# Kernel optimization log

Hardware: AMD Instinct MI355X
Metric: run time of the kernel (lower is better)

Reference implementation:

```python
import jax, jax.numpy as jnp
import numpy as np

B, N, F_IN = 32, 512, 16
H, D_HID, D_OUT = 8, 8, 32
ALPHA = 0.2
NEG = -9e15


def setup_inputs() -> dict:
    key = jax.random.key(0)
    ks = jax.random.split(key, 10)
    xv = jax.random.normal(ks[0], (B, N, F_IN), dtype=jnp.float32)
    adj = (jax.random.uniform(ks[1], (B, N, N)) < 0.05).astype(jnp.float32)
    s = 0.1
    W_heads = jax.random.normal(ks[2], (H, F_IN, D_HID), dtype=jnp.float32) * s
    a1 = jax.random.normal(ks[3], (H, D_HID), dtype=jnp.float32) * s
    a2 = jax.random.normal(ks[4], (H, D_HID), dtype=jnp.float32) * s
    W_out = jax.random.normal(ks[5], (H * D_HID, D_OUT), dtype=jnp.float32) * s
    a1_out = jax.random.normal(ks[6], (D_OUT,), dtype=jnp.float32) * s
    a2_out = jax.random.normal(ks[7], (D_OUT,), dtype=jnp.float32) * s
    W_q = jax.random.normal(ks[8], (N * D_OUT, N), dtype=jnp.float32) * s
    b_q = jax.random.normal(ks[9], (N,), dtype=jnp.float32) * s
    return {"xv": xv, "adj": adj, "W_heads": W_heads, "a1": a1, "a2": a2,
            "W_out": W_out, "a1_out": a1_out, "a2_out": a2_out,
            "W_q": W_q, "b_q": b_q}


def _masked_softmax(e, adj_mask):
    # e: [..., N, N]; adj_mask broadcastable bool
    scores = jnp.where(adj_mask, e, NEG)
    return jax.nn.softmax(scores, axis=-1)


def reference(xv, adj, W_heads, a1, a2, W_out, a1_out, a2_out, W_q, b_q):
    mask = adj > 0  # [B, N, N]
    # --- multi-head GAT layer (vectorized over batch and heads) ---
    Wh = jnp.einsum('bnf,hfd->bhnd', xv, W_heads)            # [B,H,N,Dh]
    f1 = jnp.einsum('bhnd,hd->bhn', Wh, a1)                   # a^T[:Dh] . Wh_i
    f2 = jnp.einsum('bhnd,hd->bhn', Wh, a2)                   # a^T[Dh:] . Wh_j
    e = jax.nn.leaky_relu(f1[:, :, :, None] + f2[:, :, None, :], ALPHA)  # [B,H,N,N]
    att = _masked_softmax(e, mask[:, None, :, :])
    h = jnp.einsum('bhnm,bhmd->bhnd', att, Wh)
    h = jax.nn.elu(h)                                         # concat=True heads apply elu
    h_cat = jnp.transpose(h, (0, 2, 1, 3)).reshape(B, N, H * D_HID)  # head-major concat
    # --- output attention layer (concat=False: no internal elu) ---
    Who = jnp.einsum('bnf,fd->bnd', h_cat, W_out)             # [B,N,Do]
    g1 = Who @ a1_out                                         # [B,N]
    g2 = Who @ a2_out
    eo = jax.nn.leaky_relu(g1[:, :, None] + g2[:, None, :], ALPHA)
    att_o = _masked_softmax(eo, mask)
    out = jnp.einsum('bnm,bmd->bnd', att_o, Who)
    out = jax.nn.elu(out)                                     # F.elu applied in forward
    # --- Q head ---
    q = out.reshape(B, N * D_OUT) @ W_q + b_q                 # [B,N]
    return q[..., None]                                       # [B,N,1]
```

## Files before the change

### kernel.cpp

```cpp
#include <hip/hip_runtime.h>
#include <hip/hip_bf16.h>
#include <stdint.h>


typedef unsigned long long u64;
typedef unsigned short u16;

__device__ __forceinline__ float eluf(float x) { return x > 0.f ? x : __expf(x) - 1.f; }
__device__ __forceinline__ float lrelu(float x) { return fmaxf(x, 0.2f * x); }

__device__ float g_Wh[1048576];
__device__ float g_f1[131072];
__device__ float g_f2[131072];
__device__ u64   g_mask[131072];
__device__ float g_hcat[1048576];
__device__ float g_Who[524288];
__device__ float g_g1[16384];
__device__ float g_g2[16384];
__device__ float g_out2[524288];
__device__ float g_partial[1048576];

__global__ __launch_bounds__(256) void k_mask(const float* __restrict__ adj) {
  int gw = blockIdx.x * 4 + (threadIdx.x >> 6);
  int lane = threadIdx.x & 63;
  float v = adj[(size_t)(gw >> 3) * 512 + (gw & 7) * 64 + lane];
  u64 bal = __ballot(v > 0.f);
  if (lane == 0) g_mask[gw] = bal;
}

__global__ __launch_bounds__(256) void k_wh(const float* __restrict__ xv,
                                            const float* __restrict__ whd,
                                            const float* __restrict__ a1,
                                            const float* __restrict__ a2) {
  __shared__ float w_s[128];
  __shared__ float a1s[8], a2s[8];
  int tid = threadIdx.x;
  int g = blockIdx.x * 256 + tid;
  int h = (g >> 9) & 7;
  if (tid < 128) w_s[tid] = whd[h * 128 + tid];
  if (tid < 8) { a1s[tid] = a1[h * 8 + tid]; a2s[tid] = a2[h * 8 + tid]; }
  __syncthreads();

  int b = g >> 12, n = g & 511;
  const float4* xp = (const float4*)(xv + (size_t)(b * 512 + n) * 16);
  float x[16];
#pragma unroll
  for (int i = 0; i < 4; ++i) {
    float4 v = xp[i];
    x[4 * i] = v.x; x[4 * i + 1] = v.y; x[4 * i + 2] = v.z; x[4 * i + 3] = v.w;
  }

  float wh[8] = {0, 0, 0, 0, 0, 0, 0, 0};
#pragma unroll
  for (int f = 0; f < 16; ++f) {
    float xf = x[f];
#pragma unroll
    for (int d = 0; d < 8; ++d) wh[d] += xf * w_s[f * 8 + d];
  }
  float s1 = 0.f, s2 = 0.f;
#pragma unroll
  for (int d = 0; d < 8; ++d) { s1 += wh[d] * a1s[d]; s2 += wh[d] * a2s[d]; }

  float* dst = g_Wh + (size_t)g * 8;
  *(float4*)dst = make_float4(wh[0], wh[1], wh[2], wh[3]);
  *(float4*)(dst + 4) = make_float4(wh[4], wh[5], wh[6], wh[7]);
  g_f1[g] = s1;
  g_f2[g] = s2;
}

__global__ __launch_bounds__(512) void k_gat() {
  __shared__ float wh_s[4096];
  __shared__ float f2s[512];

  int bh = blockIdx.x;
  int b = bh >> 3, h = bh & 7;
  int tid = threadIdx.x;

  {
    const float4* src = (const float4*)(g_Wh + (size_t)bh * 4096);
    float4* dst = (float4*)wh_s;
    dst[tid] = src[tid];
    dst[tid + 512] = src[tid + 512];
    f2s[tid] = g_f2[(size_t)bh * 512 + tid];
  }
  float f1v = g_f1[(size_t)bh * 512 + tid];
  const u64* mrow = g_mask + (size_t)b * 4096 + (size_t)tid * 8;
  __syncthreads();

  float acc[8] = {0, 0, 0, 0, 0, 0, 0, 0};
  float sum = 0.f;
#pragma unroll
  for (int w = 0; w < 8; ++w) {
    u64 mq = mrow[w];
    while (mq) {
      int j = __builtin_ctzll(mq);
      mq &= mq - 1;
      int col = w * 64 + j;
      float p = __expf(lrelu(f1v + f2s[col]));
      sum += p;
      const float4* wr = (const float4*)(wh_s + col * 8);
      float4 A = wr[0], Bv = wr[1];
      acc[0] += p * A.x;  acc[1] += p * A.y;  acc[2] += p * A.z;  acc[3] += p * A.w;
      acc[4] += p * Bv.x; acc[5] += p * Bv.y; acc[6] += p * Bv.z; acc[7] += p * Bv.w;
    }
  }

  float rs = sum > 0.f ? 1.0f / sum : 0.f;
  float* dst = g_hcat + (size_t)(b * 512 + tid) * 64 + h * 8;
  *(float4*)dst = make_float4(eluf(acc[0] * rs), eluf(acc[1] * rs), eluf(acc[2] * rs), eluf(acc[3] * rs));
  *(float4*)(dst + 4) = make_float4(eluf(acc[4] * rs), eluf(acc[5] * rs), eluf(acc[6] * rs), eluf(acc[7] * rs));
}

__global__ __launch_bounds__(256) void k_who(const float* __restrict__ wout,
                                             const float* __restrict__ a1o,
                                             const float* __restrict__ a2o) {
  __shared__ float wo_s[2048];
  __shared__ float a1s[32], a2s[32];
  int tid = threadIdx.x;
  for (int i = tid; i < 2048; i += 256) wo_s[i] = wout[i];
  if (tid < 32) { a1s[tid] = a1o[tid]; a2s[tid] = a2o[tid]; }
  __syncthreads();

  int g = blockIdx.x * 256 + tid;
  const float4* hp = (const float4*)(g_hcat + (size_t)g * 64);
  float acc[32];
#pragma unroll
  for (int d = 0; d < 32; ++d) acc[d] = 0.f;
#pragma unroll
  for (int f4 = 0; f4 < 16; ++f4) {
    float4 h4 = hp[f4];
    float hv[4] = {h4.x, h4.y, h4.z, h4.w};
#pragma unroll
    for (int k = 0; k < 4; ++k) {
      const float4* wr = (const float4*)(wo_s + (f4 * 4 + k) * 32);
      float hvk = hv[k];
#pragma unroll
      for (int d4 = 0; d4 < 8; ++d4) {
        float4 wv = wr[d4];
        acc[d4 * 4]     += hvk * wv.x;
        acc[d4 * 4 + 1] += hvk * wv.y;
        acc[d4 * 4 + 2] += hvk * wv.z;
        acc[d4 * 4 + 3] += hvk * wv.w;
      }
    }
  }
  float s1 = 0.f, s2 = 0.f;
#pragma unroll
  for (int d = 0; d < 32; ++d) { s1 += acc[d] * a1s[d]; s2 += acc[d] * a2s[d]; }

  float* wdst = g_Who + (size_t)g * 32;
#pragma unroll
  for (int d4 = 0; d4 < 8; ++d4)
    *(float4*)(wdst + d4 * 4) = make_float4(acc[d4 * 4], acc[d4 * 4 + 1], acc[d4 * 4 + 2], acc[d4 * 4 + 3]);
  g_g1[g] = s1;
  g_g2[g] = s2;
}

__global__ __launch_bounds__(512) void k_att2() {
  __shared__ float pool[9216];
  __shared__ float g2c[256];
  __shared__ u64 mask_s[512];

  int b = blockIdx.x >> 3;
  int t = blockIdx.x & 7;
  int tid = threadIdx.x;
  int w = tid >> 6;
  int l = tid & 63;

  mask_s[tid] = g_mask[(size_t)b * 4096 + t * 512 + tid];
  float g1v = g_g1[(size_t)b * 512 + t * 64 + l];

  float acc[32];
#pragma unroll
  for (int d = 0; d < 32; ++d) acc[d] = 0.f;
  float sum = 0.f;

#pragma unroll 1
  for (int c = 0; c < 2; ++c) {
    __syncthreads();
    {
      const float4* src = (const float4*)g_Who + (size_t)b * 4096;
      float4* dst = (float4*)pool;
      for (int i = tid; i < 2048; i += 512) dst[i] = src[c * 2048 + i];
      if (tid < 64) ((float4*)g2c)[tid] = ((const float4*)g_g2)[(size_t)b * 128 + c * 64 + tid];
    }
    __syncthreads();
    u64 mq = mask_s[l * 8 + c * 4 + (w >> 1)];
    uint32_t bits = (w & 1) ? (uint32_t)(mq >> 32) : (uint32_t)mq;
    while (bits) {
      int j = __builtin_ctz(bits);
      bits &= bits - 1;
      float p = __expf(lrelu(g1v + g2c[w * 32 + j]));
      sum += p;
      const float4* wq = (const float4*)(pool + (w * 32 + j) * 32);
#pragma unroll
      for (int d4 = 0; d4 < 8; ++d4) {
        float4 v = wq[d4];
        acc[d4 * 4]     += p * v.x;
        acc[d4 * 4 + 1] += p * v.y;
        acc[d4 * 4 + 2] += p * v.z;
        acc[d4 * 4 + 3] += p * v.w;
      }
    }
  }

#pragma unroll 1
  for (int step = 4; step >= 1; step >>= 1) {
    __syncthreads();
    if (w >= step && w < 2 * step) {
      float* rp = pool + (size_t)((w - step) * 64 + l) * 36;
#pragma unroll
      for (int d4 = 0; d4 < 8; ++d4)
        *(float4*)(rp + d4 * 4) = make_float4(acc[d4 * 4], acc[d4 * 4 + 1], acc[d4 * 4 + 2], acc[d4 * 4 + 3]);
      rp[32] = sum;
    }
    __syncthreads();
    if (w < step) {
      const float* rp = pool + (size_t)(w * 64 + l) * 36;
#pragma unroll
      for (int d = 0; d < 32; ++d) acc[d] += rp[d];
      sum += rp[32];
    }
  }

  if (w == 0) {
    float rs = sum > 0.f ? 1.0f / sum : 0.f;
    float* dst = g_out2 + (size_t)(b * 512 + t * 64 + l) * 32;
#pragma unroll
    for (int d4 = 0; d4 < 8; ++d4)
      *(float4*)(dst + d4 * 4) = make_float4(eluf(acc[d4 * 4] * rs), eluf(acc[d4 * 4 + 1] * rs),
                                             eluf(acc[d4 * 4 + 2] * rs), eluf(acc[d4 * 4 + 3] * rs));
  }
}

__global__ __launch_bounds__(256) void k_qpart(const float* __restrict__ Wq) {
  __shared__ float outT[256 * 36];
  int s = blockIdx.x >> 3;
  int c = blockIdx.x & 7;
  int tid = threadIdx.x;
  int np = c * 64 + (tid & 63);
  int bg = tid >> 6;

  for (int idx = tid; idx < 8192; idx += 256) {
    int bb = idx >> 8, kk = idx & 255;
    outT[kk * 36 + bb] = g_out2[(size_t)bb * 16384 + s * 256 + kk];
  }
  __syncthreads();

  float acc[8] = {0, 0, 0, 0, 0, 0, 0, 0};
  const float* wp = Wq + (size_t)(s * 256) * 512 + np;
  for (int kk = 0; kk < 256; ++kk) {
    float wv = wp[(size_t)kk * 512];
    const float4* op = (const float4*)(outT + kk * 36 + bg * 8);
    float4 o1 = op[0], o2 = op[1];
    acc[0] += o1.x * wv; acc[1] += o1.y * wv; acc[2] += o1.z * wv; acc[3] += o1.w * wv;
    acc[4] += o2.x * wv; acc[5] += o2.y * wv; acc[6] += o2.z * wv; acc[7] += o2.w * wv;
  }
#pragma unroll
  for (int j = 0; j < 8; ++j)
    g_partial[(size_t)(s * 32 + bg * 8 + j) * 512 + np] = acc[j];
}

__global__ __launch_bounds__(256) void k_qred(const float* __restrict__ bq,
                                              float* __restrict__ out) {
  int g = blockIdx.x * 256 + threadIdx.x;
  int b = g >> 9, np = g & 511;
  float q = bq[np];
  for (int s = 0; s < 64; ++s) q += g_partial[(size_t)(s * 32 + b) * 512 + np];
  out[g] = q;
}

extern "C" void kernel_launch(void* const* d_in, const int* in_sizes, int n_in,
                              void* d_out, int out_size, void* d_ws, size_t ws_size,
                              hipStream_t stream) {
  const float* xv = (const float*)d_in[0];
  const float* adj = (const float*)d_in[1];
  const float* W_heads = (const float*)d_in[2];
  const float* a1 = (const float*)d_in[3];
  const float* a2 = (const float*)d_in[4];
  const float* W_out = (const float*)d_in[5];
  const float* a1_out = (const float*)d_in[6];
  const float* a2_out = (const float*)d_in[7];
  const float* W_q = (const float*)d_in[8];
  const float* b_q = (const float*)d_in[9];

  k_mask<<<32768, 256, 0, stream>>>(adj);
  k_wh<<<512, 256, 0, stream>>>(xv, W_heads, a1, a2);
  k_gat<<<256, 512, 0, stream>>>();
  k_who<<<64, 256, 0, stream>>>(W_out, a1_out, a2_out);
  k_att2<<<256, 512, 0, stream>>>();
  k_qpart<<<512, 256, 0, stream>>>(W_q);
  k_qred<<<64, 256, 0, stream>>>(b_q, (float*)d_out);
}
```

Measured before the change: 188.8 us.

## Fuse Wh projection into GAT kernel, pad LDS rows, restructure mask and Q kernels

The per-head Wh projection is computed inside the GAT attention kernel, which drops the separate k_wh launch and the global round-trip through g_Wh, g_f1 and g_f2. Wh rows in LDS are padded to stride 10, and the Who rows in k_att2 to stride 36, to reduce bank conflicts. k_mask now handles 16 segments per wave, cutting its grid from 32768 to 2048 blocks. k_who runs 256 blocks of 64 threads instead of 64 blocks of 256. k_qpart drops its LDS transpose and reads g_out2 directly with wave-uniform addressing, which risks less coalesced global loads.

```diff
diff --git a/kernel.cpp b/kernel.cpp
--- a/kernel.cpp
+++ b/kernel.cpp
@@ -1,17 +1,12 @@
 #include <hip/hip_runtime.h>
-#include <hip/hip_bf16.h>
 #include <stdint.h>
 
 
 typedef unsigned long long u64;
-typedef unsigned short u16;
 
 __device__ __forceinline__ float eluf(float x) { return x > 0.f ? x : __expf(x) - 1.f; }
 __device__ __forceinline__ float lrelu(float x) { return fmaxf(x, 0.2f * x); }
 
-__device__ float g_Wh[1048576];
-__device__ float g_f1[131072];
-__device__ float g_f2[131072];
 __device__ u64   g_mask[131072];
 __device__ float g_hcat[1048576];
 __device__ float g_Who[524288];
@@ -21,35 +16,41 @@
 __device__ float g_partial[1048576];
 
 __global__ __launch_bounds__(256) void k_mask(const float* __restrict__ adj) {
-  int gw = blockIdx.x * 4 + (threadIdx.x >> 6);
+  int wid = blockIdx.x * 4 + (threadIdx.x >> 6);
   int lane = threadIdx.x & 63;
-  float v = adj[(size_t)(gw >> 3) * 512 + (gw & 7) * 64 + lane];
-  u64 bal = __ballot(v > 0.f);
-  if (lane == 0) g_mask[gw] = bal;
-}
-
-__global__ __launch_bounds__(256) void k_wh(const float* __restrict__ xv,
-                                            const float* __restrict__ whd,
-                                            const float* __restrict__ a1,
-                                            const float* __restrict__ a2) {
+#pragma unroll
+  for (int seg = 0; seg < 16; ++seg) {
+    int gw = wid * 16 + seg;
+    float v = adj[(size_t)(gw >> 3) * 512 + (gw & 7) * 64 + lane];
+    u64 bal = __ballot(v > 0.f);
+    if (lane == 0) g_mask[gw] = bal;
+  }
+}
+
+__global__ __launch_bounds__(512) void k_gat(const float* __restrict__ xv,
+                                             const float* __restrict__ whd,
+                                             const float* __restrict__ a1,
+                                             const float* __restrict__ a2) {
   __shared__ float w_s[128];
   __shared__ float a1s[8], a2s[8];
-  int tid = threadIdx.x;
-  int g = blockIdx.x * 256 + tid;
-  int h = (g >> 9) & 7;
+  __shared__ float wh_s[5120];
+  __shared__ float f2s[512];
+
+  int bh = blockIdx.x;
+  int b = bh >> 3, h = bh & 7;
+  int tid = threadIdx.x;
+
   if (tid < 128) w_s[tid] = whd[h * 128 + tid];
   if (tid < 8) { a1s[tid] = a1[h * 8 + tid]; a2s[tid] = a2[h * 8 + tid]; }
   __syncthreads();
 
-  int b = g >> 12, n = g & 511;
-  const float4* xp = (const float4*)(xv + (size_t)(b * 512 + n) * 16);
+  const float4* xp = (const float4*)(xv + (size_t)(b * 512 + tid) * 16);
   float x[16];
 #pragma unroll
   for (int i = 0; i < 4; ++i) {
     float4 v = xp[i];
     x[4 * i] = v.x; x[4 * i + 1] = v.y; x[4 * i + 2] = v.z; x[4 * i + 3] = v.w;
   }
-
   float wh[8] = {0, 0, 0, 0, 0, 0, 0, 0};
 #pragma unroll
   for (int f = 0; f < 16; ++f) {
@@ -57,33 +58,13 @@
 #pragma unroll
     for (int d = 0; d < 8; ++d) wh[d] += xf * w_s[f * 8 + d];
   }
-  float s1 = 0.f, s2 = 0.f;
-#pragma unroll
-  for (int d = 0; d < 8; ++d) { s1 += wh[d] * a1s[d]; s2 += wh[d] * a2s[d]; }
-
-  float* dst = g_Wh + (size_t)g * 8;
-  *(float4*)dst = make_float4(wh[0], wh[1], wh[2], wh[3]);
-  *(float4*)(dst + 4) = make_float4(wh[4], wh[5], wh[6], wh[7]);
-  g_f1[g] = s1;
-  g_f2[g] = s2;
-}
-
-__global__ __launch_bounds__(512) void k_gat() {
-  __shared__ float wh_s[4096];
-  __shared__ float f2s[512];
-
-  int bh = blockIdx.x;
-  int b = bh >> 3, h = bh & 7;
-  int tid = threadIdx.x;
-
-  {
-    const float4* src = (const float4*)(g_Wh + (size_t)bh * 4096);
-    float4* dst = (float4*)wh_s;
-    dst[tid] = src[tid];
-    dst[tid + 512] = src[tid + 512];
-    f2s[tid] = g_f2[(size_t)bh * 512 + tid];
-  }
-  float f1v = g_f1[(size_t)bh * 512 + tid];
+  float f1v = 0.f, s2 = 0.f;
+#pragma unroll
+  for (int d = 0; d < 8; ++d) { f1v += wh[d] * a1s[d]; s2 += wh[d] * a2s[d]; }
+  f2s[tid] = s2;
+#pragma unroll
+  for (int k = 0; k < 4; ++k)
+    *(float2*)(wh_s + tid * 10 + 2 * k) = make_float2(wh[2 * k], wh[2 * k + 1]);
   const u64* mrow = g_mask + (size_t)b * 4096 + (size_t)tid * 8;
   __syncthreads();
 
@@ -98,10 +79,13 @@
       int col = w * 64 + j;
       float p = __expf(lrelu(f1v + f2s[col]));
       sum += p;
-      const float4* wr = (const float4*)(wh_s + col * 8);
-      float4 A = wr[0], Bv = wr[1];
-      acc[0] += p * A.x;  acc[1] += p * A.y;  acc[2] += p * A.z;  acc[3] += p * A.w;
-      acc[4] += p * Bv.x; acc[5] += p * Bv.y; acc[6] += p * Bv.z; acc[7] += p * Bv.w;
+      const float* wr = wh_s + col * 10;
+      float2 A = *(const float2*)(wr);
+      float2 Bv = *(const float2*)(wr + 2);
+      float2 C = *(const float2*)(wr + 4);
+      float2 D = *(const float2*)(wr + 6);
+      acc[0] += p * A.x;  acc[1] += p * A.y;  acc[2] += p * Bv.x; acc[3] += p * Bv.y;
+      acc[4] += p * C.x;  acc[5] += p * C.y;  acc[6] += p * D.x;  acc[7] += p * D.y;
     }
   }
 
@@ -111,17 +95,17 @@
   *(float4*)(dst + 4) = make_float4(eluf(acc[4] * rs), eluf(acc[5] * rs), eluf(acc[6] * rs), eluf(acc[7] * rs));
 }
 
-__global__ __launch_bounds__(256) void k_who(const float* __restrict__ wout,
-                                             const float* __restrict__ a1o,
-                                             const float* __restrict__ a2o) {
+__global__ __launch_bounds__(64) void k_who(const float* __restrict__ wout,
+                                            const float* __restrict__ a1o,
+                                            const float* __restrict__ a2o) {
   __shared__ float wo_s[2048];
   __shared__ float a1s[32], a2s[32];
   int tid = threadIdx.x;
-  for (int i = tid; i < 2048; i += 256) wo_s[i] = wout[i];
+  for (int i = tid; i < 2048; i += 64) wo_s[i] = wout[i];
   if (tid < 32) { a1s[tid] = a1o[tid]; a2s[tid] = a2o[tid]; }
   __syncthreads();
 
-  int g = blockIdx.x * 256 + tid;
+  int g = blockIdx.x * 64 + tid;
   const float4* hp = (const float4*)(g_hcat + (size_t)g * 64);
   float acc[32];
 #pragma unroll
@@ -180,8 +164,10 @@
     __syncthreads();
     {
       const float4* src = (const float4*)g_Who + (size_t)b * 4096;
-      float4* dst = (float4*)pool;
-      for (int i = tid; i < 2048; i += 512) dst[i] = src[c * 2048 + i];
+      for (int i = tid; i < 2048; i += 512) {
+        int m = i >> 3, d4 = i & 7;
+        *(float4*)(pool + m * 36 + d4 * 4) = src[c * 2048 + i];
+      }
       if (tid < 64) ((float4*)g2c)[tid] = ((const float4*)g_g2)[(size_t)b * 128 + c * 64 + tid];
     }
     __syncthreads();
@@ -192,10 +178,10 @@
       bits &= bits - 1;
       float p = __expf(lrelu(g1v + g2c[w * 32 + j]));
       sum += p;
-      const float4* wq = (const float4*)(pool + (w * 32 + j) * 32);
+      const float* wq = pool + (w * 32 + j) * 36;
 #pragma unroll
       for (int d4 = 0; d4 < 8; ++d4) {
-        float4 v = wq[d4];
+        float4 v = *(const float4*)(wq + d4 * 4);
         acc[d4 * 4]     += p * v.x;
         acc[d4 * 4 + 1] += p * v.y;
         acc[d4 * 4 + 2] += p * v.z;
@@ -234,27 +220,22 @@
 }
 
 __global__ __launch_bounds__(256) void k_qpart(const float* __restrict__ Wq) {
-  __shared__ float outT[256 * 36];
   int s = blockIdx.x >> 3;
   int c = blockIdx.x & 7;
   int tid = threadIdx.x;
   int np = c * 64 + (tid & 63);
-  int bg = tid >> 6;
-
-  for (int idx = tid; idx < 8192; idx += 256) {
-    int bb = idx >> 8, kk = idx & 255;
-    outT[kk * 36 + bb] = g_out2[(size_t)bb * 16384 + s * 256 + kk];
-  }
-  __syncthreads();
+  int bg = __builtin_amdgcn_readfirstlane(tid >> 6);
+
+  const float* o0 = g_out2 + (size_t)(bg * 8) * 16384 + s * 256;
+  const float* wp = Wq + (size_t)(s * 256) * 512 + np;
 
   float acc[8] = {0, 0, 0, 0, 0, 0, 0, 0};
-  const float* wp = Wq + (size_t)(s * 256) * 512 + np;
+#pragma unroll 4
   for (int kk = 0; kk < 256; ++kk) {
     float wv = wp[(size_t)kk * 512];
-    const float4* op = (const float4*)(outT + kk * 36 + bg * 8);
-    float4 o1 = op[0], o2 = op[1];
-    acc[0] += o1.x * wv; acc[1] += o1.y * wv; acc[2] += o1.z * wv; acc[3] += o1.w * wv;
-    acc[4] += o2.x * wv; acc[5] += o2.y * wv; acc[6] += o2.z * wv; acc[7] += o2.w * wv;
+#pragma unroll
+    for (int j = 0; j < 8; ++j)
+      acc[j] += o0[j * 16384 + kk] * wv;
   }
 #pragma unroll
   for (int j = 0; j < 8; ++j)
@@ -284,10 +265,9 @@
   const float* W_q = (const float*)d_in[8];
   const float* b_q = (const float*)d_in[9];
 
-  k_mask<<<32768, 256, 0, stream>>>(adj);
-  k_wh<<<512, 256, 0, stream>>>(xv, W_heads, a1, a2);
-  k_gat<<<256, 512, 0, stream>>>();
-  k_who<<<64, 256, 0, stream>>>(W_out, a1_out, a2_out);
+  k_mask<<<2048, 256, 0, stream>>>(adj);
+  k_gat<<<256, 512, 0, stream>>>(xv, W_heads, a1, a2);
+  k_who<<<256, 64, 0, stream>>>(W_out, a1_out, a2_out);
   k_att2<<<256, 512, 0, stream>>>();
   k_qpart<<<512, 256, 0, stream>>>(W_q);
   k_qred<<<64, 256, 0, stream>>>(b_q, (float*)d_out);
```

Measured after the change: 211.8 us. 1.12x slower.
